# Kernel optimization log

Hardware: AMD Instinct MI355X
Metric: run time of the kernel (lower is better)

Reference implementation:

```python
import jax, jax.numpy as jnp
import numpy as np
import math

B, T, D = 2, 4096, 1024
HD = D // 2                      # head_dim
DEPTH = 12
LAMBDA_INIT = 0.8 - 0.6 * math.exp(-0.3 * DEPTH)
SCALING = HD ** -0.5
EPS = 1e-5


def setup_inputs() -> dict:
    key = jax.random.key(0)
    ks = jax.random.split(key, 11)
    f32 = jnp.float32
    return {
        "q": jax.random.normal(ks[0], (B, T, D), f32),
        "k": jax.random.normal(ks[1], (B, T, D), f32),
        "v": jax.random.normal(ks[2], (B, T, D), f32),
        "Wq": jax.random.normal(ks[3], (D, D), f32) * 0.02,
        "Wk": jax.random.normal(ks[4], (HD, D), f32) * 0.02,
        "Wv": jax.random.normal(ks[5], (D, D), f32) * 0.02,
        "Wo": jax.random.normal(ks[6], (D, D), f32) * 0.02,
        "lambda_q1": jax.random.normal(ks[7], (HD,), f32) * 0.1,
        "lambda_k1": jax.random.normal(ks[8], (HD,), f32) * 0.1,
        "lambda_q2": jax.random.normal(ks[9], (HD,), f32) * 0.1,
        "lambda_k2": jax.random.normal(ks[10], (HD,), f32) * 0.1,
    }


def reference(q, k, v, Wq, Wk, Wv, Wo, lambda_q1, lambda_k1, lambda_q2, lambda_k2):
    b, t, d = q.shape
    s = k.shape[1]
    # projections (Linear with no bias: x @ W.T)
    qp = (q @ Wq.T).reshape(b, t, 2, HD).transpose(0, 2, 1, 3) * SCALING  # [b,2,t,hd]
    kp = k @ Wk.T                                                          # [b,s,hd] (shared by both score heads)
    # dual score maps + softmax over src
    scores = jnp.einsum("bhtd,bsd->bhts", qp, kp)                          # [b,2,t,s]
    scores = jax.nn.softmax(scores.astype(jnp.float32), axis=-1).astype(qp.dtype)
    # lambda-weighted subtraction
    lam1 = jnp.exp(jnp.sum(lambda_q1 * lambda_k1))
    lam2 = jnp.exp(jnp.sum(lambda_q2 * lambda_k2))
    lam = lam1 - lam2 + LAMBDA_INIT
    attn_w = scores[:, 0] - lam * scores[:, 1]                             # [b,t,s]
    # value matmul
    vp = v @ Wv.T                                                          # [b,s,d]
    attn = jnp.einsum("bts,bsd->btd", attn_w, vp)                          # [b,t,d]
    # RMSNorm over last dim (2*head_dim == d), no affine
    rms = jax.lax.rsqrt(jnp.mean(jnp.square(attn), axis=-1, keepdims=True) + EPS)
    attn = attn * rms * (1.0 - LAMBDA_INIT)
    return attn @ Wo.T
```

## Files before the change

kernel.cpp:

```cpp
#include <hip/hip_runtime.h>
#include <stdint.h>
#include <stddef.h>

#define T_   4096
#define BT_  8192
#define SCALING_F      0.04419417382415922f
#define LAMBDA_INIT_F  0.7836057665316212f
#define ONE_MINUS_LI_F 0.2163942334683788f

typedef __attribute__((ext_vector_type(8))) short short8;
typedef __attribute__((ext_vector_type(4))) short short4v;
typedef __attribute__((ext_vector_type(4))) float f32x4;
typedef __attribute__((ext_vector_type(16))) float f32x16;

__device__ __forceinline__ short f2bf(float f){
  uint32_t u = __float_as_uint(f);
  uint32_t r = (u + 0x7fffu + ((u >> 16) & 1u)) >> 16;
  return (short)(uint16_t)r;
}

__device__ __forceinline__ f32x4 mfma16(short8 a, short8 b, f32x4 c){
  return __builtin_amdgcn_mfma_f32_16x16x32_bf16(a, b, c, 0, 0, 0);
}

__device__ __forceinline__ f32x16 mfma32(short8 a, short8 b, f32x16 c){
  return __builtin_amdgcn_mfma_f32_32x32x16_bf16(a, b, c, 0, 0, 0);
}

__device__ __forceinline__ void stage16(short* lds, const short* g){
  __builtin_amdgcn_global_load_lds(
      (const __attribute__((address_space(1))) void*)g,
      (__attribute__((address_space(3))) void*)lds, 16, 0, 0);
}

struct CvtArgs {
  const float* src[7];
  short*       dst[7];
  int          n4[7];
  int          total4;
};

__global__ void k_cvt(CvtArgs a){
  int i  = blockIdx.x*blockDim.x + threadIdx.x;
  int st = gridDim.x*blockDim.x;
  for (; i < a.total4; i += st){
    int seg = 0, off = i;
    #pragma unroll
    for (int s = 0; s < 6; s++){
      if (off >= a.n4[seg]){ off -= a.n4[seg]; seg++; }
    }
    float4 v = ((const float4*)a.src[seg])[off];
    short4v o;
    o.x = f2bf(v.x); o.y = f2bf(v.y); o.z = f2bf(v.z); o.w = f2bf(v.w);
    ((short4v*)a.dst[seg])[off] = o;
  }
}

template<int EPI>
__global__ __launch_bounds__(256, 3) void k_gemm(const short* __restrict__ A,
                                                 const short* __restrict__ Bm,
                                                 void* __restrict__ Cp, int ldc){
  __shared__ short As[128*32];
  __shared__ short Bs[128*32];
  const int tid = threadIdx.x;
  const int w = tid >> 6, l = tid & 63;
  const int m0 = blockIdx.x * 128;
  const int n0 = blockIdx.y * 128;
  const int wr = w >> 1, wc = w & 1;

  f32x4 acc[4][4] = {};

  const short* gA = A  + (size_t)(m0 + w*32 + (l>>2))*1024 + (l&3)*8;
  const short* gB = Bm + (size_t)(n0 + w*32 + (l>>2))*1024 + (l&3)*8;

  for (int k0 = 0; k0 < 1024; k0 += 32){
    stage16(As + w*1024,       gA + k0);
    stage16(As + w*1024 + 512, gA + 16*1024 + k0);
    stage16(Bs + w*1024,       gB + k0);
    stage16(Bs + w*1024 + 512, gB + 16*1024 + k0);
    __syncthreads();
    short8 aF[4], bF[4];
    #pragma unroll
    for (int i = 0; i < 4; i++){
      aF[i] = *(const short8*)&As[(wr*64 + i*16 + (l&15))*32 + (l>>4)*8];
      bF[i] = *(const short8*)&Bs[(wc*64 + i*16 + (l&15))*32 + (l>>4)*8];
    }
    #pragma unroll
    for (int i = 0; i < 4; i++)
      #pragma unroll
      for (int j = 0; j < 4; j++)
        acc[i][j] = mfma16(aF[i], bF[j], acc[i][j]);
    __syncthreads();
  }

  #pragma unroll
  for (int i = 0; i < 4; i++){
    #pragma unroll
    for (int j = 0; j < 4; j++){
      const size_t r0 = (size_t)m0 + wr*64 + i*16 + (l>>4)*4;
      const size_t c  = (size_t)n0 + wc*64 + j*16 + (l&15);
      #pragma unroll
      for (int rg = 0; rg < 4; rg++){
        float v = acc[i][j][rg];
        if (EPI == 2){
          ((float*)Cp)[(r0+rg)*(size_t)ldc + c] = v;
        } else {
          if (EPI == 1) v *= SCALING_F;
          ((short*)Cp)[(r0+rg)*(size_t)ldc + c] = f2bf(v);
        }
      }
    }
  }
}

__global__ __launch_bounds__(512, 2) void k_attn(
    const short* __restrict__ QP, const short* __restrict__ KP,
    const short* __restrict__ VPT,
    const float* __restrict__ lq1, const float* __restrict__ lk1,
    const float* __restrict__ lq2, const float* __restrict__ lk2,
    short* __restrict__ Ab)
{
  __shared__ short Ks[64*512];
  __shared__ short Qs[32*1024];
  __shared__ short Pl[2][32][72];
  __shared__ float lsum[8][16];
  __shared__ float rinv[2][32];
  __shared__ float ssq[8][32];

  int wg = blockIdx.x;
  wg = (wg & 7)*32 + (wg >> 3);
  const int b  = wg >> 7;
  const int t0 = (wg & 127) * 32;

  const int tid = threadIdx.x;
  const int w = tid >> 6, l = tid & 63;

  const int rc = w >> 1, h = rc >> 1, tch = rc & 1, scb = w & 1;

  f32x16 acc[2][4] = {};
  float lacc[4] = {0.f,0.f,0.f,0.f};

  const short* kpb = KP  + (size_t)(b*T_)*512;
  const short* vbp = VPT + (size_t)(w*128 + (l&31))*BT_ + (size_t)b*T_ + (l>>5)*8;

  const int jx = (l >> 4) ^ (l & 3);
  const int kx = (l >> 2) & 1;

  {
    const short* qsrc = QP + (size_t)(b*T_ + t0)*1024;
    #pragma unroll
    for (int j = 0; j < 4; j++){
      int r = w*4 + j;
      #pragma unroll
      for (int h2 = 0; h2 < 2; h2++)
        stage16(&Qs[r*1024 + h2*512],
                qsrc + (size_t)r*1024 + (h2*64 + (l ^ (r & 7)))*8);
    }
    #pragma unroll
    for (int j = 0; j < 8; j++)
      stage16(&Ks[(w*8 + j)*512], kpb + (size_t)(w*8 + j)*512 + ((l ^ j)*8));
  }
  __syncthreads();

  const short* qp0 = &Qs[(tch*16 + (l&15))*1024 + h*512 + jx*8];
  const short* kp0 = &Ks[(scb*32 + (l&15))*512 + jx*8];
  const short* kp1 = kp0 + 16*512;

  for (int st = 0; st < 64; st++){
    const int s0 = st*64;

    short8 varr[16];
    #pragma unroll
    for (int dt = 0; dt < 4; dt++)
      #pragma unroll
      for (int ks = 0; ks < 4; ks++)
        varr[dt*4 + ks] = *(const short8*)(vbp + (size_t)dt*32*BT_ + s0 + ks*16);
    __builtin_amdgcn_sched_barrier(0);

    f32x4 sa0 = {0.f,0.f,0.f,0.f}, sa1 = {0.f,0.f,0.f,0.f};
    #pragma unroll
    for (int kk = 0; kk < 16; kk++){
      const int ko = ((kk ^ kx) << 5);
      short8 qf = *(const short8*)(qp0 + ko);
      short8 b0 = *(const short8*)(kp0 + ko);
      short8 b1 = *(const short8*)(kp1 + ko);
      sa0 = mfma16(qf, b0, sa0);
      sa1 = mfma16(qf, b1, sa1);
    }

    #pragma unroll
    for (int rg = 0; rg < 4; rg++){
      float e0 = __expf(sa0[rg]);
      float e1 = __expf(sa1[rg]);
      lacc[rg] += e0 + e1;
      int row = tch*16 + (l>>4)*4 + rg;
      Pl[h][row][(2*scb+0)*16 + (l&15)] = f2bf(e0);
      Pl[h][row][(2*scb+1)*16 + (l&15)] = f2bf(e1);
    }

    asm volatile("s_waitcnt lgkmcnt(0)" ::: "memory");
    __builtin_amdgcn_s_barrier();

    if (st + 1 < 64){
      const short* ksrc = kpb + (size_t)((st+1)*64 + w*8)*512;
      #pragma unroll
      for (int j = 0; j < 8; j++)
        stage16(&Ks[(w*8 + j)*512], ksrc + (size_t)j*512 + ((l ^ j)*8));
    }

    #pragma unroll
    for (int ks = 0; ks < 4; ks++){
      short8 pa0 = *(const short8*)&Pl[0][l&31][ks*16 + (l>>5)*8];
      short8 pa1 = *(const short8*)&Pl[1][l&31][ks*16 + (l>>5)*8];
      #pragma unroll
      for (int dt = 0; dt < 4; dt++){
        acc[0][dt] = mfma32(pa0, varr[dt*4 + ks], acc[0][dt]);
        acc[1][dt] = mfma32(pa1, varr[dt*4 + ks], acc[1][dt]);
      }
    }

    __syncthreads();
  }

  float s1 = 0.f, s2 = 0.f;
  #pragma unroll
  for (int i = 0; i < 8; i++){
    int idx = l*8 + i;
    s1 += lq1[idx]*lk1[idx];
    s2 += lq2[idx]*lk2[idx];
  }
  #pragma unroll
  for (int off = 1; off < 64; off <<= 1){
    s1 += __shfl_xor(s1, off, 64);
    s2 += __shfl_xor(s2, off, 64);
  }
  const float lam = __expf(s1) - __expf(s2) + LAMBDA_INIT_F;

  #pragma unroll
  for (int off = 1; off < 16; off <<= 1)
    #pragma unroll
    for (int rg = 0; rg < 4; rg++) lacc[rg] += __shfl_xor(lacc[rg], off, 16);
  if ((l & 15) == 0){
    #pragma unroll
    for (int rg = 0; rg < 4; rg++) lsum[w][(l>>4)*4 + rg] = lacc[rg];
  }
  __syncthreads();
  if (tid < 64){
    int hh = tid >> 5, t = tid & 31;
    int rcc = hh*2 + (t >> 4), ric = t & 15;
    rinv[hh][t] = 1.0f / (lsum[rcc*2][ric] + lsum[rcc*2+1][ric]);
  }
  __syncthreads();

  float ps[16];
  #pragma unroll
  for (int reg = 0; reg < 16; reg++) ps[reg] = 0.f;
  #pragma unroll
  for (int dt = 0; dt < 4; dt++){
    #pragma unroll
    for (int reg = 0; reg < 16; reg++){
      int t = (reg&3) + 8*(reg>>2) + 4*(l>>5);
      float o = acc[0][dt][reg]*rinv[0][t] - lam*acc[1][dt][reg]*rinv[1][t];
      ps[reg] += o*o;
    }
  }
  #pragma unroll
  for (int off = 1; off < 32; off <<= 1)
    #pragma unroll
    for (int reg = 0; reg < 16; reg++) ps[reg] += __shfl_xor(ps[reg], off, 64);
  if ((l & 31) == 0){
    #pragma unroll
    for (int reg = 0; reg < 16; reg++){
      int t = (reg&3) + 8*(reg>>2) + 4*(l>>5);
      ssq[w][t] = ps[reg];
    }
  }
  __syncthreads();

  #pragma unroll
  for (int reg = 0; reg < 16; reg++){
    int t = (reg&3) + 8*(reg>>2) + 4*(l>>5);
    float tot = 0.f;
    #pragma unroll
    for (int w8 = 0; w8 < 8; w8++) tot += ssq[w8][t];
    float scale = rsqrtf(tot*(1.0f/1024.0f) + 1e-5f) * ONE_MINUS_LI_F;
    short* orow = Ab + (size_t)(b*T_ + t0 + t)*1024 + w*128 + (l&31);
    #pragma unroll
    for (int dt = 0; dt < 4; dt++){
      float o = acc[0][dt][reg]*rinv[0][t] - lam*acc[1][dt][reg]*rinv[1][t];
      orow[dt*32] = f2bf(o*scale);
    }
  }
}

extern "C" void kernel_launch(void* const* d_in, const int* in_sizes, int n_in,
                              void* d_out, int out_size, void* d_ws, size_t ws_size,
                              hipStream_t stream){
  const float* q   = (const float*)d_in[0];
  const float* k   = (const float*)d_in[1];
  const float* v   = (const float*)d_in[2];
  const float* Wq  = (const float*)d_in[3];
  const float* Wk  = (const float*)d_in[4];
  const float* Wv  = (const float*)d_in[5];
  const float* Wo  = (const float*)d_in[6];
  const float* lq1 = (const float*)d_in[7];
  const float* lk1 = (const float*)d_in[8];
  const float* lq2 = (const float*)d_in[9];
  const float* lk2 = (const float*)d_in[10];

  short* ws   = (short*)d_ws;
  short* qb   = ws;
  short* kb   = qb  + (size_t)8192*1024;
  short* vb   = kb  + (size_t)8192*1024;
  short* Wqb  = vb  + (size_t)8192*1024;
  short* Wkb  = Wqb + (size_t)1024*1024;
  short* Wvb  = Wkb + (size_t)512*1024;
  short* Wob  = Wvb + (size_t)1024*1024;
  short* QPb  = Wob + (size_t)1024*1024;
  short* KPb  = QPb + (size_t)8192*1024;
  short* VPTb = KPb + (size_t)8192*512;
  short* Ab   = qb;

  CvtArgs ca;
  ca.src[0]=q;  ca.dst[0]=qb;  ca.n4[0]=(8192*1024)/4;
  ca.src[1]=k;  ca.dst[1]=kb;  ca.n4[1]=(8192*1024)/4;
  ca.src[2]=v;  ca.dst[2]=vb;  ca.n4[2]=(8192*1024)/4;
  ca.src[3]=Wq; ca.dst[3]=Wqb; ca.n4[3]=(1024*1024)/4;
  ca.src[4]=Wk; ca.dst[4]=Wkb; ca.n4[4]=(512*1024)/4;
  ca.src[5]=Wv; ca.dst[5]=Wvb; ca.n4[5]=(1024*1024)/4;
  ca.src[6]=Wo; ca.dst[6]=Wob; ca.n4[6]=(1024*1024)/4;
  ca.total4 = ca.n4[0]+ca.n4[1]+ca.n4[2]+ca.n4[3]+ca.n4[4]+ca.n4[5]+ca.n4[6];
  k_cvt<<<2048, 256, 0, stream>>>(ca);

  k_gemm<1><<<dim3(64, 8), 256, 0, stream>>>(qb, Wqb, QPb, 1024);
  k_gemm<0><<<dim3(64, 4), 256, 0, stream>>>(kb, Wkb, KPb, 512);
  k_gemm<0><<<dim3(8, 64), 256, 0, stream>>>(Wvb, vb, VPTb, 8192);
  k_attn<<<dim3(256), 512, 0, stream>>>(QPb, KPb, VPTb, lq1, lk1, lq2, lk2, Ab);
  k_gemm<2><<<dim3(64, 8), 256, 0, stream>>>(Ab, Wob, d_out, 1024);
}
```

Measured before the change: 481.3 us.

## Replace fused attention with materialized exp-score GEMM plus dual PV GEMM

Result: no change. 486.3 us (+1.0%).

```diff
diff --git a/kernel.cpp b/kernel.cpp
--- a/kernel.cpp
+++ b/kernel.cpp
@@ -31,6 +31,30 @@
   __builtin_amdgcn_global_load_lds(
       (const __attribute__((address_space(1))) void*)g,
       (__attribute__((address_space(3))) void*)lds, 16, 0, 0);
+}
+
+__global__ void k_zero(float* p, int n){
+  int i = blockIdx.x*blockDim.x + threadIdx.x;
+  if (i < n) p[i] = 0.f;
+}
+
+__global__ void k_lam(const float* __restrict__ lq1, const float* __restrict__ lk1,
+                      const float* __restrict__ lq2, const float* __restrict__ lk2,
+                      float* __restrict__ out){
+  int l = threadIdx.x & 63;
+  float s1 = 0.f, s2 = 0.f;
+  #pragma unroll
+  for (int i = 0; i < 8; i++){
+    int idx = l*8 + i;
+    s1 += lq1[idx]*lk1[idx];
+    s2 += lq2[idx]*lk2[idx];
+  }
+  #pragma unroll
+  for (int off = 1; off < 64; off <<= 1){
+    s1 += __shfl_xor(s1, off, 64);
+    s2 += __shfl_xor(s2, off, 64);
+  }
+  if (l == 0) out[0] = __expf(s1) - __expf(s2) + LAMBDA_INIT_F;
 }
 
 struct CvtArgs {
@@ -57,9 +81,12 @@
 }
 
 template<int EPI>
-__global__ __launch_bounds__(256, 3) void k_gemm(const short* __restrict__ A,
-                                                 const short* __restrict__ Bm,
-                                                 void* __restrict__ Cp, int ldc){
+__global__ __launch_bounds__(256, 3) void k_gemm(
+    const short* __restrict__ A, int lda,
+    const short* __restrict__ Bm, int ldb,
+    void* __restrict__ Cp, int ldc, int K,
+    float* __restrict__ aux)
+{
   __shared__ short As[128*32];
   __shared__ short Bs[128*32];
   const int tid = threadIdx.x;
@@ -68,16 +95,26 @@
   const int n0 = blockIdx.y * 128;
   const int wr = w >> 1, wc = w & 1;
 
+  const short* Ae = A;
+  short* Ceb = (short*)Cp;
+  float* auxe = aux;
+  if (EPI == 4){
+    const int hz = blockIdx.z;
+    Ae   += (size_t)hz * 512;
+    Ceb  += (size_t)hz * 4096 * 4096;
+    auxe += (size_t)hz * 4096;
+  }
+
   f32x4 acc[4][4] = {};
 
-  const short* gA = A  + (size_t)(m0 + w*32 + (l>>2))*1024 + (l&3)*8;
-  const short* gB = Bm + (size_t)(n0 + w*32 + (l>>2))*1024 + (l&3)*8;
-
-  for (int k0 = 0; k0 < 1024; k0 += 32){
+  const short* gA = Ae + (size_t)(m0 + w*32 + (l>>2))*lda + (l&3)*8;
+  const short* gB = Bm + (size_t)(n0 + w*32 + (l>>2))*ldb + (l&3)*8;
+
+  for (int k0 = 0; k0 < K; k0 += 32){
     stage16(As + w*1024,       gA + k0);
-    stage16(As + w*1024 + 512, gA + 16*1024 + k0);
+    stage16(As + w*1024 + 512, gA + (size_t)16*lda + k0);
     stage16(Bs + w*1024,       gB + k0);
-    stage16(Bs + w*1024 + 512, gB + 16*1024 + k0);
+    stage16(Bs + w*1024 + 512, gB + (size_t)16*ldb + k0);
     __syncthreads();
     short8 aF[4], bF[4];
     #pragma unroll
@@ -93,23 +130,147 @@
     __syncthreads();
   }
 
-  #pragma unroll
-  for (int i = 0; i < 4; i++){
-    #pragma unroll
-    for (int j = 0; j < 4; j++){
-      const size_t r0 = (size_t)m0 + wr*64 + i*16 + (l>>4)*4;
-      const size_t c  = (size_t)n0 + wc*64 + j*16 + (l&15);
-      #pragma unroll
-      for (int rg = 0; rg < 4; rg++){
-        float v = acc[i][j][rg];
-        if (EPI == 2){
-          ((float*)Cp)[(r0+rg)*(size_t)ldc + c] = v;
-        } else {
-          if (EPI == 1) v *= SCALING_F;
-          ((short*)Cp)[(r0+rg)*(size_t)ldc + c] = f2bf(v);
+  if (EPI == 4){
+    float rs[4][4];
+    #pragma unroll
+    for (int i = 0; i < 4; i++)
+      #pragma unroll
+      for (int rg = 0; rg < 4; rg++) rs[i][rg] = 0.f;
+    #pragma unroll
+    for (int i = 0; i < 4; i++){
+      #pragma unroll
+      for (int j = 0; j < 4; j++){
+        const size_t r0 = (size_t)m0 + wr*64 + i*16 + (l>>4)*4;
+        const size_t c  = (size_t)n0 + wc*64 + j*16 + (l&15);
+        #pragma unroll
+        for (int rg = 0; rg < 4; rg++){
+          float e = __expf(acc[i][j][rg]);
+          Ceb[(r0+rg)*(size_t)ldc + c] = f2bf(e);
+          rs[i][rg] += e;
         }
       }
     }
+    #pragma unroll
+    for (int off = 1; off < 16; off <<= 1)
+      #pragma unroll
+      for (int i = 0; i < 4; i++)
+        #pragma unroll
+        for (int rg = 0; rg < 4; rg++) rs[i][rg] += __shfl_xor(rs[i][rg], off, 16);
+    if ((l & 15) == 0){
+      #pragma unroll
+      for (int i = 0; i < 4; i++)
+        #pragma unroll
+        for (int rg = 0; rg < 4; rg++)
+          atomicAdd(&auxe[m0 + wr*64 + i*16 + (l>>4)*4 + rg], rs[i][rg]);
+    }
+  } else {
+    #pragma unroll
+    for (int i = 0; i < 4; i++){
+      #pragma unroll
+      for (int j = 0; j < 4; j++){
+        const size_t r0 = (size_t)m0 + wr*64 + i*16 + (l>>4)*4;
+        const size_t c  = (size_t)n0 + wc*64 + j*16 + (l&15);
+        #pragma unroll
+        for (int rg = 0; rg < 4; rg++){
+          float v = acc[i][j][rg];
+          if (EPI == 2){
+            ((float*)Cp)[(r0+rg)*(size_t)ldc + c] = v;
+          } else if (EPI == 3){
+            float sc = rsqrtf(auxe[r0+rg]*(1.0f/1024.0f) + 1e-5f) * ONE_MINUS_LI_F;
+            ((float*)Cp)[(r0+rg)*(size_t)ldc + c] = v * sc;
+          } else {
+            if (EPI == 1) v *= SCALING_F;
+            ((short*)Cp)[(r0+rg)*(size_t)ldc + c] = f2bf(v);
+          }
+        }
+      }
+    }
+  }
+}
+
+__global__ __launch_bounds__(512, 2) void k_pv(
+    const short* __restrict__ E1, const short* __restrict__ E2,
+    const short* __restrict__ Bm,
+    short* __restrict__ Cp,
+    const float* __restrict__ ls1, const float* __restrict__ ls2,
+    float* __restrict__ ssq, const float* __restrict__ lamp)
+{
+  __shared__ short As1[2][128*32];
+  __shared__ short As2[2][128*32];
+  __shared__ short Bs [2][128*32];
+  const int tid = threadIdx.x;
+  const int w = tid >> 6, l = tid & 63;
+  const int m0 = blockIdx.x * 128;
+  const int n0 = blockIdx.y * 128;
+  const int wr = w >> 1, wc = w & 1;
+
+  f32x4 acc1[2][4] = {}, acc2[2][4] = {};
+
+  const short* gA1 = E1 + (size_t)(m0 + w*16 + (l>>2))*4096 + (l&3)*8;
+  const short* gA2 = E2 + (size_t)(m0 + w*16 + (l>>2))*4096 + (l&3)*8;
+  const short* gB  = Bm + (size_t)(n0 + w*16 + (l>>2))*8192 + (l&3)*8;
+
+  stage16(As1[0] + w*512, gA1);
+  stage16(As2[0] + w*512, gA2);
+  stage16(Bs [0] + w*512, gB);
+  __syncthreads();
+
+  for (int k0 = 0; k0 < 4096; k0 += 32){
+    const int cur = (k0 >> 5) & 1;
+    if (k0 + 32 < 4096){
+      stage16(As1[cur^1] + w*512, gA1 + k0 + 32);
+      stage16(As2[cur^1] + w*512, gA2 + k0 + 32);
+      stage16(Bs [cur^1] + w*512, gB  + k0 + 32);
+    }
+    short8 a1[2], a2[2], bF[4];
+    #pragma unroll
+    for (int i = 0; i < 2; i++){
+      a1[i] = *(const short8*)&As1[cur][(wr*32 + i*16 + (l&15))*32 + (l>>4)*8];
+      a2[i] = *(const short8*)&As2[cur][(wr*32 + i*16 + (l&15))*32 + (l>>4)*8];
+    }
+    #pragma unroll
+    for (int j = 0; j < 4; j++)
+      bF[j] = *(const short8*)&Bs[cur][(wc*64 + j*16 + (l&15))*32 + (l>>4)*8];
+    #pragma unroll
+    for (int i = 0; i < 2; i++)
+      #pragma unroll
+      for (int j = 0; j < 4; j++){
+        acc1[i][j] = mfma16(a1[i], bF[j], acc1[i][j]);
+        acc2[i][j] = mfma16(a2[i], bF[j], acc2[i][j]);
+      }
+    __syncthreads();
+  }
+
+  const float lam = lamp[0];
+  float ps[2][4] = {};
+  #pragma unroll
+  for (int i = 0; i < 2; i++){
+    #pragma unroll
+    for (int rg = 0; rg < 4; rg++){
+      const int r = m0 + wr*32 + i*16 + (l>>4)*4 + rg;
+      const float ri1 = 1.0f / ls1[r];
+      const float ri2 = 1.0f / ls2[r];
+      #pragma unroll
+      for (int j = 0; j < 4; j++){
+        const int c = n0 + wc*64 + j*16 + (l&15);
+        float o = acc1[i][j][rg]*ri1 - lam*acc2[i][j][rg]*ri2;
+        Cp[(size_t)r*1024 + c] = f2bf(o);
+        ps[i][rg] += o*o;
+      }
+    }
+  }
+  #pragma unroll
+  for (int off = 1; off < 16; off <<= 1)
+    #pragma unroll
+    for (int i = 0; i < 2; i++)
+      #pragma unroll
+      for (int rg = 0; rg < 4; rg++) ps[i][rg] += __shfl_xor(ps[i][rg], off, 16);
+  if ((l & 15) == 0){
+    #pragma unroll
+    for (int i = 0; i < 2; i++)
+      #pragma unroll
+      for (int rg = 0; rg < 4; rg++)
+        atomicAdd(&ssq[m0 + wr*32 + i*16 + (l>>4)*4 + rg], ps[i][rg]);
   }
 }
 
@@ -134,7 +295,6 @@
 
   const int tid = threadIdx.x;
   const int w = tid >> 6, l = tid & 63;
-
   const int rc = w >> 1, h = rc >> 1, tch = rc & 1, scb = w & 1;
 
   f32x16 acc[2][4] = {};
@@ -308,33 +468,89 @@
   const float* lq2 = (const float*)d_in[9];
   const float* lk2 = (const float*)d_in[10];
 
-  short* ws   = (short*)d_ws;
-  short* qb   = ws;
-  short* kb   = qb  + (size_t)8192*1024;
-  short* vb   = kb  + (size_t)8192*1024;
-  short* Wqb  = vb  + (size_t)8192*1024;
-  short* Wkb  = Wqb + (size_t)1024*1024;
-  short* Wvb  = Wkb + (size_t)512*1024;
-  short* Wob  = Wvb + (size_t)1024*1024;
-  short* QPb  = Wob + (size_t)1024*1024;
-  short* KPb  = QPb + (size_t)8192*1024;
-  short* VPTb = KPb + (size_t)8192*512;
-  short* Ab   = qb;
-
-  CvtArgs ca;
-  ca.src[0]=q;  ca.dst[0]=qb;  ca.n4[0]=(8192*1024)/4;
-  ca.src[1]=k;  ca.dst[1]=kb;  ca.n4[1]=(8192*1024)/4;
-  ca.src[2]=v;  ca.dst[2]=vb;  ca.n4[2]=(8192*1024)/4;
-  ca.src[3]=Wq; ca.dst[3]=Wqb; ca.n4[3]=(1024*1024)/4;
-  ca.src[4]=Wk; ca.dst[4]=Wkb; ca.n4[4]=(512*1024)/4;
-  ca.src[5]=Wv; ca.dst[5]=Wvb; ca.n4[5]=(1024*1024)/4;
-  ca.src[6]=Wo; ca.dst[6]=Wob; ca.n4[6]=(1024*1024)/4;
-  ca.total4 = ca.n4[0]+ca.n4[1]+ca.n4[2]+ca.n4[3]+ca.n4[4]+ca.n4[5]+ca.n4[6];
-  k_cvt<<<2048, 256, 0, stream>>>(ca);
-
-  k_gemm<1><<<dim3(64, 8), 256, 0, stream>>>(qb, Wqb, QPb, 1024);
-  k_gemm<0><<<dim3(64, 4), 256, 0, stream>>>(kb, Wkb, KPb, 512);
-  k_gemm<0><<<dim3(8, 64), 256, 0, stream>>>(Wvb, vb, VPTb, 8192);
-  k_attn<<<dim3(256), 512, 0, stream>>>(QPb, KPb, VPTb, lq1, lk1, lq2, lk2, Ab);
-  k_gemm<2><<<dim3(64, 8), 256, 0, stream>>>(Ab, Wob, d_out, 1024);
-}
+  short* ws = (short*)d_ws;
+  const size_t M1 = 1u << 20;
+  const size_t NEED = (size_t)62 * M1 * 2;
+
+  if (ws_size >= NEED){
+    short* Wob  = ws;
+    short* QPb  = ws + 1*M1;
+    short* KPb  = ws + 9*M1;
+    short* VPTb = ws + 13*M1;
+    short* AbP  = ws + 21*M1;
+    float* stats= (float*)(ws + 29*M1);
+    float* lsum = stats;
+    float* ssqb = stats + 16384;
+    float* lamb = stats + 24576;
+    short* Ebuf = ws + 30*M1;
+    short* qb   = ws + 30*M1;
+    short* kb   = ws + 38*M1;
+    short* vb   = ws + 46*M1;
+    short* Wqb  = ws + 54*M1;
+    short* Wkb  = ws + 55*M1;
+    short* Wvb  = ws + 55*M1 + (M1>>1);
+
+    k_zero<<<96, 256, 0, stream>>>(stats, 24576);
+    k_lam<<<1, 64, 0, stream>>>(lq1, lk1, lq2, lk2, lamb);
+
+    CvtArgs ca;
+    ca.src[0]=q;  ca.dst[0]=qb;  ca.n4[0]=(8192*1024)/4;
+    ca.src[1]=k;  ca.dst[1]=kb;  ca.n4[1]=(8192*1024)/4;
+    ca.src[2]=v;  ca.dst[2]=vb;  ca.n4[2]=(8192*1024)/4;
+    ca.src[3]=Wq; ca.dst[3]=Wqb; ca.n4[3]=(1024*1024)/4;
+    ca.src[4]=Wk; ca.dst[4]=Wkb; ca.n4[4]=(512*1024)/4;
+    ca.src[5]=Wv; ca.dst[5]=Wvb; ca.n4[5]=(1024*1024)/4;
+    ca.src[6]=Wo; ca.dst[6]=Wob; ca.n4[6]=(1024*1024)/4;
+    ca.total4 = ca.n4[0]+ca.n4[1]+ca.n4[2]+ca.n4[3]+ca.n4[4]+ca.n4[5]+ca.n4[6];
+    k_cvt<<<2048, 256, 0, stream>>>(ca);
+
+    k_gemm<1><<<dim3(64, 8), 256, 0, stream>>>(qb,1024,  Wqb,1024, QPb, 1024, 1024, nullptr);
+    k_gemm<0><<<dim3(64, 4), 256, 0, stream>>>(kb,1024,  Wkb,1024, KPb,  512, 1024, nullptr);
+    k_gemm<0><<<dim3(8, 64), 256, 0, stream>>>(Wvb,1024, vb,1024,  VPTb,8192, 1024, nullptr);
+
+    for (int b = 0; b < 2; b++){
+      k_gemm<4><<<dim3(32, 32, 2), 256, 0, stream>>>(
+          QPb + (size_t)b*4096*1024, 1024,
+          KPb + (size_t)b*4096*512,  512,
+          Ebuf, 4096, 512,
+          lsum + (size_t)b*2*4096);
+      k_pv<<<dim3(32, 8), 512, 0, stream>>>(
+          Ebuf, Ebuf + (size_t)16*M1,
+          VPTb + (size_t)b*4096,
+          AbP + (size_t)b*4096*1024,
+          lsum + (size_t)(b*2+0)*4096, lsum + (size_t)(b*2+1)*4096,
+          ssqb + (size_t)b*4096, lamb);
+    }
+
+    k_gemm<3><<<dim3(64, 8), 256, 0, stream>>>(AbP,1024, Wob,1024, d_out, 1024, 1024, ssqb);
+  } else {
+    short* qb   = ws;
+    short* kb   = qb  + (size_t)8192*1024;
+    short* vb   = kb  + (size_t)8192*1024;
+    short* Wqb  = vb  + (size_t)8192*1024;
+    short* Wkb  = Wqb + (size_t)1024*1024;
+    short* Wvb  = Wkb + (size_t)512*1024;
+    short* Wob  = Wvb + (size_t)1024*1024;
+    short* QPb  = Wob + (size_t)1024*1024;
+    short* KPb  = QPb + (size_t)8192*1024;
+    short* VPTb = KPb + (size_t)8192*512;
+    short* Ab   = qb;
+
+    CvtArgs ca;
+    ca.src[0]=q;  ca.dst[0]=qb;  ca.n4[0]=(8192*1024)/4;
+    ca.src[1]=k;  ca.dst[1]=kb;  ca.n4[1]=(8192*1024)/4;
+    ca.src[2]=v;  ca.dst[2]=vb;  ca.n4[2]=(8192*1024)/4;
+    ca.src[3]=Wq; ca.dst[3]=Wqb; ca.n4[3]=(1024*1024)/4;
+    ca.src[4]=Wk; ca.dst[4]=Wkb; ca.n4[4]=(512*1024)/4;
+    ca.src[5]=Wv; ca.dst[5]=Wvb; ca.n4[5]=(1024*1024)/4;
+    ca.src[6]=Wo; ca.dst[6]=Wob; ca.n4[6]=(1024*1024)/4;
+    ca.total4 = ca.n4[0]+ca.n4[1]+ca.n4[2]+ca.n4[3]+ca.n4[4]+ca.n4[5]+ca.n4[6];
+    k_cvt<<<2048, 256, 0, stream>>>(ca);
+
+    k_gemm<1><<<dim3(64, 8), 256, 0, stream>>>(qb,1024,  Wqb,1024, QPb, 1024, 1024, nullptr);
+    k_gemm<0><<<dim3(64, 4), 256, 0, stream>>>(kb,1024,  Wkb,1024, KPb,  512, 1024, nullptr);
+    k_gemm<0><<<dim3(8, 64), 256, 0, stream>>>(Wvb,1024, vb,1024,  VPTb,8192, 1024, nullptr);
+    k_attn<<<dim3(256), 512, 0, stream>>>(QPb, KPb, VPTb, lq1, lk1, lq2, lk2, Ab);
+    k_gemm<2><<<dim3(64, 8), 256, 0, stream>>>(Ab,1024, Wob,1024, d_out, 1024, 1024, nullptr);
+  }
+}
```
